# Performance work log

Hardware: AMD Instinct MI355X
Metric: run time of the kernel (lower is better)

## Reference

```python
import jax, jax.numpy as jnp
import numpy as np

DIM = 256        # word / relation / entity-type embedding dim
STATEDIM = 256   # agent state dim
VOCAB = 100000
REL_COUNT = 25
T = 128          # sentence length


def _lstm(wvs, Wih, Whh, bih, bhh, reverse):
    # PyTorch LSTMCell gate order: i, f, g, o
    def step(carry, x):
        h, c = carry
        g = x @ Wih.T + bih + h @ Whh.T + bhh
        i, f, gg, o = jnp.split(g, 4)
        c = jax.nn.sigmoid(f) * c + jax.nn.sigmoid(i) * jnp.tanh(gg)
        h = jax.nn.sigmoid(o) * jnp.tanh(c)
        return (h, c), h
    init = (jnp.zeros((DIM,), jnp.float32), jnp.zeros((DIM,), jnp.float32))
    _, hs = jax.lax.scan(step, init, wvs, reverse=reverse)
    return hs


def setup_inputs() -> dict:
    key = jax.random.key(0)
    ks = jax.random.split(key, 32)
    def p(i, shape, scale=0.05):
        return (jax.random.normal(ks[i], shape) * scale).astype(jnp.float32)
    return {
        "text": jax.random.randint(ks[0], (T,), 0, VOCAB, dtype=jnp.int32),
        "wordvector": p(1, (VOCAB, DIM)),
        "relvec": p(2, (REL_COUNT + 1, DIM)),
        "entvec": p(3, (7, DIM)),
        "WihL": p(4, (4 * DIM, DIM)), "WhhL": p(5, (4 * DIM, DIM)),
        "bihL": p(6, (4 * DIM,)), "bhhL": p(7, (4 * DIM,)),
        "WihR": p(8, (4 * DIM, DIM)), "WhhR": p(9, (4 * DIM, DIM)),
        "bihR": p(10, (4 * DIM,)), "bhhR": p(11, (4 * DIM,)),
        "Wt": p(12, (STATEDIM, 3 * DIM + STATEDIM)), "bt": p(13, (STATEDIM,)),
        "Wp": p(14, (REL_COUNT + 1, STATEDIM)), "bp": p(15, (REL_COUNT + 1,)),
        "Wb": p(16, (STATEDIM, 3 * DIM + 2 * STATEDIM)), "bb": p(17, (STATEDIM,)),
        "Wpl": p(18, (REL_COUNT, 7, STATEDIM)), "bpl": p(19, (REL_COUNT, 7)),
        "Wtt": p(20, (STATEDIM, STATEDIM)), "btt": p(21, (STATEDIM,)),
        "Wtb": p(22, (STATEDIM, STATEDIM)), "btb": p(23, (STATEDIM,)),
        "Wbt": p(24, (STATEDIM, STATEDIM)), "bbt": p(25, (STATEDIM,)),
    }


def reference(text, wordvector, relvec, entvec, WihL, WhhL, bihL, bhhL,
              WihR, WhhR, bihR, bhhR, Wt, bt, Wp, bp, Wb, bb, Wpl, bpl,
              Wtt, btt, Wtb, btb, Wbt, bbt):
    # mode = "test_NER": deterministic argmax sampling, dropout disabled.
    wvs = wordvector[text]                               # [T, DIM]
    front = _lstm(wvs, WihL, WhhL, bihL, bhhL, False)    # [T, DIM]
    back = _lstm(wvs, WihR, WhhR, bihR, bhhR, True)      # [T, DIM]
    wordin = jnp.concatenate([front, back], axis=1)      # [T, 2*DIM]

    def bot_rollout(rel_idx, target, memb0):
        Wr, br = Wpl[rel_idx], bpl[rel_idx]              # per-relation head
        def stepb(carry, w):
            memb, ab = carry
            inpb = jnp.concatenate([w, entvec[ab], memb, target])
            outb = jnp.tanh(inpb @ Wb.T + bb)            # dropout off (test)
            probb = jax.nn.softmax(outb @ Wr.T + br)
            ab2 = jnp.argmax(probb).astype(jnp.int32)
            return (outb, ab2), (ab2, probb[ab2])
        (membf, _), (acts, aps) = jax.lax.scan(
            stepb, (memb0, jnp.zeros((), jnp.int32)), wordin)
        return membf, acts, aps

    def top_step(carry, w):
        mem, rel_action = carry
        inp = jnp.concatenate([w, relvec[rel_action], mem])
        outp = jnp.tanh(inp @ Wt.T + bt)                 # dropout off (test)
        prob = jax.nn.softmax(outp @ Wp.T + bp)
        action = jnp.argmax(prob).astype(jnp.int32)
        actprob = prob[action]
        do_ner = action > 0
        rel_next = jnp.where(do_ner, action, rel_action)
        rel_idx = jnp.maximum(action, 1) - 1
        target = outp @ Wtt.T + btt
        memb0 = outp @ Wtb.T + btb
        membf, acts, aps = bot_rollout(rel_idx, target, memb0)
        mem_after = membf @ Wbt.T + bbt
        mem_next = jnp.where(do_ner, mem_after, outp)
        acts = jnp.where(do_ner, acts, 0)
        aps = jnp.where(do_ner, aps, 0.0)
        return (mem_next, rel_next), (action, actprob, acts, aps)

    init = (jnp.zeros((STATEDIM,), jnp.float32), jnp.zeros((), jnp.int32))
    _, (top_actions, top_actprobs, bot_actions, bot_actprobs) = jax.lax.scan(
        top_step, init, wordin)
    # bot rows where no NER sub-rollout fired are zero-filled (orig: empty lists)
    return top_actions, top_actprobs, bot_actions, bot_actprobs
```

## Files before the change

### kernel.cpp

```cpp
#include <hip/hip_runtime.h>
#include <float.h>

constexpr int SEQ  = 128;
constexpr int D    = 256;
constexpr int G    = 1024;
constexpr int NREL = 26;
constexpr int NENT = 7;

__global__ void k_trans(const float* __restrict__ in, float* __restrict__ out,
                        int rows, int cols, int in_stride, int in_off)
{
    int idx = blockIdx.x * 256 + threadIdx.x;
    if (idx >= rows * cols) return;
    int i = idx % rows;
    int k = idx / rows;
    out[idx] = in[(size_t)i * in_stride + in_off + k];
}

__global__ __launch_bounds__(1024) void k_xg(
    const int* __restrict__ text, const float* __restrict__ wv,
    const float* __restrict__ Wih, const float* __restrict__ bih,
    const float* __restrict__ bhh, float* __restrict__ xg)
{
    int t = blockIdx.x, j = threadIdx.x;
    const float* x  = wv + (size_t)text[t] * D;
    const float* wr = Wih + (size_t)j * D;
    float acc = bih[j] + bhh[j];
    for (int k = 0; k < D; ++k) acc += x[k] * wr[k];
    xg[t * G + j] = acc;
}

__global__ __launch_bounds__(1024) void k_lstm(
    const float* __restrict__ xgF, const float* __restrict__ xgB,
    const float* __restrict__ WHTF, const float* __restrict__ WHTB,
    float* __restrict__ wordin)
{
    int dir = blockIdx.x;
    const float* xg  = dir ? xgB  : xgF;
    const float* WHT = dir ? WHTB : WHTF;
    __shared__ float h[D], c[D], g[G];
    int j = threadIdx.x;
    if (j < D) { h[j] = 0.f; c[j] = 0.f; }
    __syncthreads();
    for (int s = 0; s < SEQ; ++s) {
        int t = dir ? (SEQ - 1 - s) : s;
        float acc = xg[t * G + j];
        for (int k = 0; k < D; ++k) acc += WHT[k * G + j] * h[k];
        g[j] = acc;
        __syncthreads();
        if (j < D) {
            float si = 1.f / (1.f + expf(-g[j]));
            float sf = 1.f / (1.f + expf(-g[D + j]));
            float gg = tanhf(g[2 * D + j]);
            float so = 1.f / (1.f + expf(-g[3 * D + j]));
            float cn = sf * c[j] + si * gg;
            float hn = so * tanhf(cn);
            c[j] = cn; h[j] = hn;
            wordin[t * (2 * D) + dir * D + j] = hn;
        }
        __syncthreads();
    }
}

__global__ __launch_bounds__(256) void k_prep2(
    const float* __restrict__ wordin,
    const float* __restrict__ WTWT, const float* __restrict__ WBWT,
    const float* __restrict__ WTRT, const float* __restrict__ WBET,
    const float* __restrict__ relvec, const float* __restrict__ entvec,
    const float* __restrict__ btv, const float* __restrict__ bbv,
    float* __restrict__ TW, float* __restrict__ BW,
    float* __restrict__ RV, float* __restrict__ EV)
{
    int b = blockIdx.x, i = threadIdx.x;
    if (b < SEQ) {
        const float* w = wordin + b * (2 * D);
        float a1 = btv[i], a2 = bbv[i];
        for (int j = 0; j < 2 * D; ++j) {
            float wv = w[j];
            a1 += wv * WTWT[j * D + i];
            a2 += wv * WBWT[j * D + i];
        }
        TW[b * D + i] = a1;
        BW[b * D + i] = a2;
    } else if (b < SEQ + NREL) {
        int r = b - SEQ;
        const float* x = relvec + r * D;
        float a = 0.f;
        for (int k = 0; k < D; ++k) a += x[k] * WTRT[k * D + i];
        RV[r * D + i] = a;
    } else {
        int e = b - SEQ - NREL;
        const float* x = entvec + e * D;
        float a = 0.f;
        for (int k = 0; k < D; ++k) a += x[k] * WBET[k * D + i];
        EV[e * D + i] = a;
    }
}

__global__ __launch_bounds__(256) void k_m1(
    const float* __restrict__ WBGT, const float* __restrict__ Wtt,
    float* __restrict__ M1T)
{
    int j = blockIdx.x, i = threadIdx.x;
    float a = 0.f;
    for (int k = 0; k < D; ++k) a = fmaf(WBGT[k * D + i], Wtt[k * D + j], a);
    M1T[j * D + i] = a;
}

__global__ __launch_bounds__(256) void k_c1(
    const float* __restrict__ WBGT, const float* __restrict__ btt,
    float* __restrict__ c1)
{
    int i = threadIdx.x;
    float a = 0.f;
    for (int k = 0; k < D; ++k) a = fmaf(WBGT[k * D + i], btt[k], a);
    c1[i] = a;
}

__global__ __launch_bounds__(256) void k_pack(
    const float* __restrict__ Wb, float* __restrict__ WB2)
{
    int e = blockIdx.x * 256 + threadIdx.x;
    int tid = e >> 7, kk = e & 127;
    int h = tid >> 8, i = tid & 255;
    WB2[e] = Wb[(size_t)i * (5 * D) + 3 * D + h * 128 + kk];
}

__device__ inline float mv_half(const float* __restrict__ Wcol,
                                const float* __restrict__ x)
{
    float a0 = 0.f, a1 = 0.f, a2 = 0.f, a3 = 0.f;
    #pragma unroll
    for (int kk = 0; kk < 128; kk += 4) {
        a0 = fmaf(Wcol[(kk + 0) * D], x[kk + 0], a0);
        a1 = fmaf(Wcol[(kk + 1) * D], x[kk + 1], a1);
        a2 = fmaf(Wcol[(kk + 2) * D], x[kk + 2], a2);
        a3 = fmaf(Wcol[(kk + 3) * D], x[kk + 3], a3);
    }
    return (a0 + a1) + (a2 + a3);
}

template<int W>
__device__ inline void grp_smax(float lv, int n, int lane, int& am, float& pm)
{
    float mx = lv;
    #pragma unroll
    for (int off = W / 2; off; off >>= 1) mx = fmaxf(mx, __shfl_xor(mx, off));
    float e  = (lane < n) ? expf(lv - mx) : 0.f;
    float se = e;
    #pragma unroll
    for (int off = W / 2; off; off >>= 1) se += __shfl_xor(se, off);
    float p  = (lane < n) ? (e / se) : -1.f;
    float q  = p;
    #pragma unroll
    for (int off = W / 2; off; off >>= 1) q = fmaxf(q, __shfl_xor(q, off));
    unsigned long long mask = __ballot(p == q);
    am = __ffsll((long long)mask) - 1;
    pm = q;
}

__global__ __launch_bounds__(512) void k_main2(
    const float* __restrict__ TW,   const float* __restrict__ BW,
    const float* __restrict__ RV,   const float* __restrict__ EV,
    const float* __restrict__ WTMT, const float* __restrict__ WTBT,
    const float* __restrict__ WBTT, const float* __restrict__ M1T,
    const float* __restrict__ c1v,  const float* __restrict__ WB2,
    const float* __restrict__ Wp,   const float* __restrict__ bp,
    const float* __restrict__ Wpl,  const float* __restrict__ bpl,
    const float* __restrict__ btb,  const float* __restrict__ bbt,
    float* __restrict__ out)
{
    const int tid  = threadIdx.x;
    const int lane = tid & 63;
    const int wv   = tid >> 6;
    const int h    = tid >> 8;
    const int i    = tid & 255;
    const bool lower = (tid < 256);

    __shared__ __align__(16) float xbuf[2][D];
    __shared__ __align__(16) float pbuf[D], pbufB[D], pbufC[D];
    __shared__ __align__(16) float mem[D], outv[D];
    __shared__ __align__(16) float Esh[NENT * D], WrSh[NENT * D];
    __shared__ float lpart[4][32];
    __shared__ float brSh[8];

    float4 wb[32];
    {
        const float4* src = reinterpret_cast<const float4*>(WB2) + tid * 32;
        #pragma unroll
        for (int q = 0; q < 32; ++q) wb[q] = src[q];
    }
    for (int k = tid; k < NENT * D; k += 512) Esh[k] = EV[k];
    if (lower) mem[i] = 0.f;
    __syncthreads();

    const float* WTMh = WTMT + (size_t)h * 128 * D + i;
    const float* WTBh = WTBT + (size_t)h * 128 * D + i;
    const float* WBTh = WBTT + (size_t)h * 128 * D + i;
    const float* M1h  = M1T  + (size_t)h * 128 * D + i;

    int rel = 0;

    for (int t = 0; t < SEQ; ++t) {
        float a = mv_half(WTMh, mem + h * 128);
        if (!lower) pbuf[i] = a;
        __syncthreads();
        if (lower) {
            float tot  = a + pbuf[i] + TW[t * D + i] + RV[rel * D + i];
            float outp = tanhf(tot);
            outv[i] = outp;
            #pragma unroll
            for (int r = 0; r < NREL; ++r) {
                float pp = outp * Wp[r * D + i];
                #pragma unroll
                for (int off = 32; off; off >>= 1) pp += __shfl_xor(pp, off);
                if (lane == 0) lpart[wv][r] = pp;
            }
        }
        __syncthreads();
        float lv = -FLT_MAX;
        if (lane < NREL)
            lv = lpart[0][lane] + lpart[1][lane] + lpart[2][lane] +
                 lpart[3][lane] + bp[lane];
        int am; float pm;
        grp_smax<32>(lv, NREL, lane, am, pm);
        if (tid == 0) { out[t] = (float)am; out[SEQ + t] = pm; }
        const int action = am;

        if (action > 0) {
            rel = action;
            float bs = mv_half(WTBh, outv + h * 128);
            float cs = mv_half(M1h,  outv + h * 128);
            if (!lower) { pbufB[i] = bs; pbufC[i] = cs; }
            const size_t wbase = (size_t)(action - 1) * NENT * D;
            for (int k = tid; k < NENT * D; k += 512) WrSh[k] = Wpl[wbase + k];
            if (tid < NENT) brSh[tid] = bpl[(action - 1) * NENT + tid];
            __syncthreads();
            float btm = 0.f;
            if (lower) {
                xbuf[0][i] = bs + pbufB[i] + btb[i];
                btm = cs + pbufC[i] + c1v[i];
            }
            __syncthreads();

            int p = 0, ab = 0;
            for (int s = 0; s < SEQ; ++s) {
                const float4* xb =
                    reinterpret_cast<const float4*>(xbuf[p] + h * 128);
                float m0 = 0.f, m1 = 0.f, m2 = 0.f, m3 = 0.f;
                #pragma unroll
                for (int q = 0; q < 32; q += 4) {
                    float4 x0 = xb[q], x1 = xb[q + 1], x2 = xb[q + 2], x3 = xb[q + 3];
                    m0 = fmaf(wb[q].x,     x0.x, m0); m0 = fmaf(wb[q].y,     x0.y, m0);
                    m0 = fmaf(wb[q].z,     x0.z, m0); m0 = fmaf(wb[q].w,     x0.w, m0);
                    m1 = fmaf(wb[q + 1].x, x1.x, m1); m1 = fmaf(wb[q + 1].y, x1.y, m1);
                    m1 = fmaf(wb[q + 1].z, x1.z, m1); m1 = fmaf(wb[q + 1].w, x1.w, m1);
                    m2 = fmaf(wb[q + 2].x, x2.x, m2); m2 = fmaf(wb[q + 2].y, x2.y, m2);
                    m2 = fmaf(wb[q + 2].z, x2.z, m2); m2 = fmaf(wb[q + 2].w, x2.w, m2);
                    m3 = fmaf(wb[q + 3].x, x3.x, m3); m3 = fmaf(wb[q + 3].y, x3.y, m3);
                    m3 = fmaf(wb[q + 3].z, x3.z, m3); m3 = fmaf(wb[q + 3].w, x3.w, m3);
                }
                float ms = (m0 + m1) + (m2 + m3);
                if (!lower) pbuf[i] = ms;
                __syncthreads();
                if (lower) {
                    float tot = ms + pbuf[i] + BW[s * D + i] +
                                Esh[ab * D + i] + btm;
                    float ob = tanhf(tot);
                    xbuf[p ^ 1][i] = ob;
                    #pragma unroll
                    for (int r = 0; r < NENT; ++r) {
                        float pp = ob * WrSh[r * D + i];
                        #pragma unroll
                        for (int off = 32; off; off >>= 1)
                            pp += __shfl_xor(pp, off);
                        if (lane == 0) lpart[wv][r] = pp;
                    }
                }
                __syncthreads();
                float lv2 = -FLT_MAX;
                if (lane < NENT)
                    lv2 = lpart[0][lane] + lpart[1][lane] + lpart[2][lane] +
                          lpart[3][lane] + brSh[lane];
                int am2; float pm2;
                grp_smax<8>(lv2, NENT, lane, am2, pm2);
                if (tid == 0) {
                    out[2 * SEQ + t * SEQ + s] = (float)am2;
                    out[2 * SEQ + SEQ * SEQ + t * SEQ + s] = pm2;
                }
                ab = am2;
                p ^= 1;
            }
            float es = mv_half(WBTh, xbuf[p] + h * 128);
            if (!lower) pbuf[i] = es;
            __syncthreads();
            if (lower) mem[i] = es + pbuf[i] + bbt[i];
            __syncthreads();
        } else {
            if (lower) mem[i] = outv[i];
            if (tid < SEQ) {
                out[2 * SEQ + t * SEQ + tid] = 0.f;
                out[2 * SEQ + SEQ * SEQ + t * SEQ + tid] = 0.f;
            }
            __syncthreads();
        }
    }
}

extern "C" void kernel_launch(void* const* d_in, const int* in_sizes, int n_in,
                              void* d_out, int out_size, void* d_ws, size_t ws_size,
                              hipStream_t stream)
{
    (void)in_sizes; (void)n_in; (void)out_size; (void)ws_size;
    const int*   text       = (const int*)  d_in[0];
    const float* wordvector = (const float*)d_in[1];
    const float* relvec     = (const float*)d_in[2];
    const float* entvec     = (const float*)d_in[3];
    const float* WihL = (const float*)d_in[4];  const float* WhhL = (const float*)d_in[5];
    const float* bihL = (const float*)d_in[6];  const float* bhhL = (const float*)d_in[7];
    const float* WihR = (const float*)d_in[8];  const float* WhhR = (const float*)d_in[9];
    const float* bihR = (const float*)d_in[10]; const float* bhhR = (const float*)d_in[11];
    const float* Wt   = (const float*)d_in[12]; const float* bt   = (const float*)d_in[13];
    const float* Wp   = (const float*)d_in[14]; const float* bp   = (const float*)d_in[15];
    const float* Wb   = (const float*)d_in[16]; const float* bb   = (const float*)d_in[17];
    const float* Wpl  = (const float*)d_in[18]; const float* bpl  = (const float*)d_in[19];
    const float* Wtt  = (const float*)d_in[20]; const float* btt  = (const float*)d_in[21];
    const float* Wtb  = (const float*)d_in[22]; const float* btb  = (const float*)d_in[23];
    const float* Wbt  = (const float*)d_in[24]; const float* bbt  = (const float*)d_in[25];

    float* ws = (float*)d_ws;
    size_t o = 0;
    auto take = [&](size_t n) { float* p = ws + o; o += n; return p; };
    float* XGF    = take(SEQ * G);
    float* XGB    = take(SEQ * G);
    float* WHLT   = take(D * G);
    float* WHRT   = take(D * G);
    float* WORDIN = take(SEQ * 2 * D);
    float* TW     = take(SEQ * D);
    float* BW     = take(SEQ * D);
    float* RVb    = take(NREL * D);
    float* EVb    = take(NENT * D);
    float* WTWT   = take(2 * D * D);
    float* WTRT   = take(D * D);
    float* WTMT   = take(D * D);
    float* WBWT   = take(2 * D * D);
    float* WBET   = take(D * D);
    float* WBGT   = take(D * D);
    float* WTBT   = take(D * D);
    float* WBTT   = take(D * D);
    float* M1T    = take(D * D);
    float* C1     = take(D);
    float* WB2    = take(2 * 128 * D);

    auto tr = [&](const float* in, float* outp, int rows, int cols, int stride, int off) {
        int n = rows * cols;
        k_trans<<<(n + 255) / 256, 256, 0, stream>>>(in, outp, rows, cols, stride, off);
    };
    tr(WhhL, WHLT, G, D, D, 0);
    tr(WhhR, WHRT, G, D, D, 0);
    tr(Wt,  WTWT, D, 2 * D, G, 0);
    tr(Wt,  WTRT, D, D, G, 512);
    tr(Wt,  WTMT, D, D, G, 768);
    tr(Wb,  WBWT, D, 2 * D, 5 * D, 0);
    tr(Wb,  WBET, D, D, 5 * D, 512);
    tr(Wb,  WBGT, D, D, 5 * D, 1024);
    tr(Wtb, WTBT, D, D, D, 0);
    tr(Wbt, WBTT, D, D, D, 0);

    k_m1<<<D, D, 0, stream>>>(WBGT, Wtt, M1T);
    k_c1<<<1, D, 0, stream>>>(WBGT, btt, C1);
    k_pack<<<256, 256, 0, stream>>>(Wb, WB2);

    k_xg<<<SEQ, 1024, 0, stream>>>(text, wordvector, WihL, bihL, bhhL, XGF);
    k_xg<<<SEQ, 1024, 0, stream>>>(text, wordvector, WihR, bihR, bhhR, XGB);
    k_lstm<<<2, 1024, 0, stream>>>(XGF, XGB, WHLT, WHRT, WORDIN);
    k_prep2<<<SEQ + NREL + NENT, 256, 0, stream>>>(WORDIN, WTWT, WBWT, WTRT, WBET,
                                                   relvec, entvec, bt, bb,
                                                   TW, BW, RVb, EVb);
    k_main2<<<1, 512, 0, stream>>>(TW, BW, RVb, EVb, WTMT, WTBT, WBTT, M1T, C1,
                                   WB2, Wp, bp, Wpl, bpl, btb, bbt,
                                   (float*)d_out);
}
```

Baseline: 61.99 ms.

## Use packed FMA in bottom recurrence, keep entity vectors in registers, prefetch BW

The inner bottom-rollout matvec now uses two-wide vector FMAs on register-resident weights, so the compiler can emit packed fp32 FMA instructions. The entity embedding table moves from shared memory into seven per-thread registers, picked with a select chain. The next BW row is loaded one step early to hide global-load latency on the serial critical path, and launch bounds now request two blocks per SM. Together these raise register pressure, and the launch bound may cause spills of the 128-register weight cache.

```diff
diff --git a/kernel.cpp b/kernel.cpp
--- a/kernel.cpp
+++ b/kernel.cpp
@@ -6,6 +6,8 @@
 constexpr int G    = 1024;
 constexpr int NREL = 26;
 constexpr int NENT = 7;
+
+typedef float v2f __attribute__((ext_vector_type(2)));
 
 __global__ void k_trans(const float* __restrict__ in, float* __restrict__ out,
                         int rows, int cols, int in_stride, int in_off)
@@ -159,7 +161,7 @@
     pm = q;
 }
 
-__global__ __launch_bounds__(512) void k_main2(
+__global__ __launch_bounds__(512, 2) void k_main2(
     const float* __restrict__ TW,   const float* __restrict__ BW,
     const float* __restrict__ RV,   const float* __restrict__ EV,
     const float* __restrict__ WTMT, const float* __restrict__ WTBT,
@@ -180,18 +182,24 @@
     __shared__ __align__(16) float xbuf[2][D];
     __shared__ __align__(16) float pbuf[D], pbufB[D], pbufC[D];
     __shared__ __align__(16) float mem[D], outv[D];
-    __shared__ __align__(16) float Esh[NENT * D], WrSh[NENT * D];
+    __shared__ __align__(16) float WrSh[NENT * D];
     __shared__ float lpart[4][32];
     __shared__ float brSh[8];
 
-    float4 wb[32];
+    v2f w2[64];
     {
-        const float4* src = reinterpret_cast<const float4*>(WB2) + tid * 32;
+        const v2f* src = reinterpret_cast<const v2f*>(WB2) + tid * 64;
         #pragma unroll
-        for (int q = 0; q < 32; ++q) wb[q] = src[q];
-    }
-    for (int k = tid; k < NENT * D; k += 512) Esh[k] = EV[k];
-    if (lower) mem[i] = 0.f;
+        for (int q = 0; q < 64; ++q) w2[q] = src[q];
+    }
+    float ev0 = 0.f, ev1 = 0.f, ev2 = 0.f, ev3 = 0.f,
+          ev4 = 0.f, ev5 = 0.f, ev6 = 0.f;
+    if (lower) {
+        ev0 = EV[0 * D + i]; ev1 = EV[1 * D + i]; ev2 = EV[2 * D + i];
+        ev3 = EV[3 * D + i]; ev4 = EV[4 * D + i]; ev5 = EV[5 * D + i];
+        ev6 = EV[6 * D + i];
+        mem[i] = 0.f;
+    }
     __syncthreads();
 
     const float* WTMh = WTMT + (size_t)h * 128 * D + i;
@@ -236,10 +244,11 @@
             for (int k = tid; k < NENT * D; k += 512) WrSh[k] = Wpl[wbase + k];
             if (tid < NENT) brSh[tid] = bpl[(action - 1) * NENT + tid];
             __syncthreads();
-            float btm = 0.f;
+            float btm = 0.f, bwc = 0.f;
             if (lower) {
                 xbuf[0][i] = bs + pbufB[i] + btb[i];
                 btm = cs + pbufC[i] + c1v[i];
+                bwc = BW[i];
             }
             __syncthreads();
 
@@ -247,25 +256,27 @@
             for (int s = 0; s < SEQ; ++s) {
                 const float4* xb =
                     reinterpret_cast<const float4*>(xbuf[p] + h * 128);
-                float m0 = 0.f, m1 = 0.f, m2 = 0.f, m3 = 0.f;
+                v2f A0 = {0.f, 0.f}, A1 = {0.f, 0.f},
+                    A2 = {0.f, 0.f}, A3 = {0.f, 0.f};
                 #pragma unroll
-                for (int q = 0; q < 32; q += 4) {
-                    float4 x0 = xb[q], x1 = xb[q + 1], x2 = xb[q + 2], x3 = xb[q + 3];
-                    m0 = fmaf(wb[q].x,     x0.x, m0); m0 = fmaf(wb[q].y,     x0.y, m0);
-                    m0 = fmaf(wb[q].z,     x0.z, m0); m0 = fmaf(wb[q].w,     x0.w, m0);
-                    m1 = fmaf(wb[q + 1].x, x1.x, m1); m1 = fmaf(wb[q + 1].y, x1.y, m1);
-                    m1 = fmaf(wb[q + 1].z, x1.z, m1); m1 = fmaf(wb[q + 1].w, x1.w, m1);
-                    m2 = fmaf(wb[q + 2].x, x2.x, m2); m2 = fmaf(wb[q + 2].y, x2.y, m2);
-                    m2 = fmaf(wb[q + 2].z, x2.z, m2); m2 = fmaf(wb[q + 2].w, x2.w, m2);
-                    m3 = fmaf(wb[q + 3].x, x3.x, m3); m3 = fmaf(wb[q + 3].y, x3.y, m3);
-                    m3 = fmaf(wb[q + 3].z, x3.z, m3); m3 = fmaf(wb[q + 3].w, x3.w, m3);
+                for (int q = 0; q < 32; q += 2) {
+                    float4 x0 = xb[q], x1 = xb[q + 1];
+                    v2f xa = {x0.x, x0.y}, xc = {x0.z, x0.w};
+                    v2f xd = {x1.x, x1.y}, xe = {x1.z, x1.w};
+                    A0 = __builtin_elementwise_fma(w2[2 * q + 0], xa, A0);
+                    A1 = __builtin_elementwise_fma(w2[2 * q + 1], xc, A1);
+                    A2 = __builtin_elementwise_fma(w2[2 * q + 2], xd, A2);
+                    A3 = __builtin_elementwise_fma(w2[2 * q + 3], xe, A3);
                 }
-                float ms = (m0 + m1) + (m2 + m3);
+                float ms = ((A0.x + A0.y) + (A1.x + A1.y)) +
+                           ((A2.x + A2.y) + (A3.x + A3.y));
                 if (!lower) pbuf[i] = ms;
                 __syncthreads();
                 if (lower) {
-                    float tot = ms + pbuf[i] + BW[s * D + i] +
-                                Esh[ab * D + i] + btm;
+                    float ev = (ab == 0) ? ev0 : (ab == 1) ? ev1 :
+                               (ab == 2) ? ev2 : (ab == 3) ? ev3 :
+                               (ab == 4) ? ev4 : (ab == 5) ? ev5 : ev6;
+                    float tot = ms + pbuf[i] + bwc + ev + btm;
                     float ob = tanhf(tot);
                     xbuf[p ^ 1][i] = ob;
                     #pragma unroll
@@ -276,6 +287,8 @@
                             pp += __shfl_xor(pp, off);
                         if (lane == 0) lpart[wv][r] = pp;
                     }
+                    int sn = (s + 1 < SEQ) ? s + 1 : s;
+                    bwc = BW[sn * D + i];
                 }
                 __syncthreads();
                 float lv2 = -FLT_MAX;
```

New measurement: 60.78 ms. About the same (-2.0%).
